# Optimization experiments

Measured on AMD Instinct MI355X. Metric: run time of the kernel, lower is better.

The kernel has to match this reference:

```python
import jax, jax.numpy as jnp
import numpy as np

EPS = 1e-13

def masked_softmax(x, mask):
    # Non-memory-efficient path of the original: softmax(x*mask), re-mask, renormalize.
    p = jax.nn.softmax(x * mask, axis=-1) * mask
    return p / (jnp.sum(p, axis=-1, keepdims=True) + EPS)

def setup_inputs() -> dict:
    key = jax.random.key(0)
    ka, kb, kma, kmb = jax.random.split(key, 4)
    B, La, Lb, D = 32, 1024, 1024, 256
    a = jax.random.normal(ka, (B, La, D), dtype=jnp.float32)
    b = jax.random.normal(kb, (B, Lb, D), dtype=jnp.float32)
    mask_a = jax.random.randint(kma, (B, La, 1), 0, 2, dtype=jnp.int32)
    mask_b = jax.random.randint(kmb, (B, Lb, 1), 0, 2, dtype=jnp.int32)
    return {"a": a, "b": b, "mask_a": mask_a, "mask_b": mask_b}

def reference(a, b, mask_a, mask_b):
    # a: [B, La, D], b: [B, Lb, D], mask_a: [B, La, 1], mask_b: [B, Lb, 1]
    ma = mask_a.astype(a.dtype)  # [B, La, 1]
    mb = mask_b.astype(b.dtype)  # [B, Lb, 1]
    attn = jnp.einsum('bid,bjd->bij', a, b)            # [B, La, Lb]
    amask = ma * jnp.swapaxes(mb, 1, 2)                 # outer product mask [B, La, Lb]
    weight_for_a = masked_softmax(attn, amask)          # softmax over Lb
    attended_a = jnp.einsum('bij,bjd->bid', weight_for_a, b)  # [B, La, D]
    attn_t = jnp.swapaxes(attn, 1, 2)                   # [B, Lb, La]
    amask_t = jnp.swapaxes(amask, 1, 2)
    weight_for_b = masked_softmax(attn_t, amask_t)      # softmax over La
    attended_b = jnp.einsum('bji,bid->bjd', weight_for_b, a)  # [B, Lb, D]
    return (attended_a, attended_b)
```

## Files before the change

### kernel.cpp

```cpp
#include <hip/hip_runtime.h>
#include <math.h>
#include <stdint.h>


#define NB    32
#define SEQ   1024
#define DIM   256
#define BM    128
#define BN    64
#define SHIFT 60.0f
#define PS    1048

typedef unsigned int uint;
typedef unsigned short ushort;
typedef __attribute__((ext_vector_type(8)))  short short8;
typedef __attribute__((ext_vector_type(16))) float f32x16;

#define KC_BATCH  (64 * 1024 * 8)
#define KC_TENSOR ((size_t)NB * KC_BATCH)
#define T_BATCH   (128 * 256 * 8)
#define T_TENSOR  ((size_t)NB * T_BATCH)
#define IDX_INTS  ((size_t)NB * SEQ)
#define WS_NEED   ((2 * KC_TENSOR + 2 * T_TENSOR) * sizeof(ushort) + (2 * IDX_INTS + 64) * sizeof(int))

__device__ __forceinline__ ushort bf16_rn(float x) {
    union { float f; uint u; } v; v.f = x;
    uint r = v.u + 0x7fffu + ((v.u >> 16) & 1u);
    return (ushort)(r >> 16);
}
__device__ __forceinline__ float bf16_to_f(ushort h) {
    union { uint u; float f; } v; v.u = ((uint)h) << 16;
    return v.f;
}
__device__ __forceinline__ void gl_lds16(const ushort* g, ushort* l) {
    __builtin_amdgcn_global_load_lds(
        (const __attribute__((address_space(1))) void*)g,
        (__attribute__((address_space(3))) void*)l, 16, 0, 0);
}

__global__ __launch_bounds__(1024)
void compact(const int* __restrict__ ma, const int* __restrict__ mb,
             int* __restrict__ idxA, int* __restrict__ idxB, int* __restrict__ nvArr)
{
    const int batch = blockIdx.x;
    const int t     = blockIdx.y;
    const int* m = t ? mb : ma;
    int* idx = (t ? idxB : idxA) + batch * SEQ;
    const int tid = threadIdx.x;
    const int lane = tid & 63, wv = tid >> 6;

    __shared__ int wsum[16];
    __shared__ int base[17];

    int v = (m[batch * SEQ + tid] != 0) ? 1 : 0;
    unsigned long long bal = __ballot(v);
    int lanePre = __popcll(bal & ((1ULL << lane) - 1ULL));
    if (lane == 0) wsum[wv] = __popcll(bal);
    __syncthreads();
    if (tid == 0) {
        int acc = 0;
        #pragma unroll
        for (int w = 0; w < 16; ++w) { base[w] = acc; acc += wsum[w]; }
        base[16] = acc;
        nvArr[t * NB + batch] = acc;
    }
    __syncthreads();
    if (v) idx[base[wv] + lanePre] = tid;
    if (tid >= base[16]) idx[tid] = 0;
}

__global__ __launch_bounds__(256)
void gatherK(const float* __restrict__ A, const float* __restrict__ Bt,
             const int* __restrict__ idxA, const int* __restrict__ idxB,
             const int* __restrict__ nvArr,
             ushort* __restrict__ aKc, ushort* __restrict__ bKc)
{
    const int z     = blockIdx.z;
    const int batch = blockIdx.y;
    const int soct  = blockIdx.x;
    const float* src = z ? Bt : A;
    const int* idx = (z ? idxB : idxA) + batch * SEQ;
    const int nv = nvArr[z * NB + batch];
    ushort* kcb = (z ? bKc : aKc) + (size_t)batch * KC_BATCH;

    const int tid = threadIdx.x;
    const int oct = tid >> 3, srow = tid & 7;
    const int c = soct * 8 + srow;

    float xs[8] = {0.f, 0.f, 0.f, 0.f, 0.f, 0.f, 0.f, 0.f};
    if (c < nv) {
        const float* rp = src + ((size_t)batch * SEQ + idx[c]) * DIM + oct * 8;
        float4 x0 = *(const float4*)rp;
        float4 x1 = *(const float4*)(rp + 4);
        xs[0]=x0.x; xs[1]=x0.y; xs[2]=x0.z; xs[3]=x0.w;
        xs[4]=x1.x; xs[5]=x1.y; xs[6]=x1.z; xs[7]=x1.w;
    }
    short8 hv, lv;
    #pragma unroll
    for (int j = 0; j < 8; ++j) {
        ushort h = bf16_rn(xs[j]);
        hv[j] = (short)h;
        lv[j] = (short)bf16_rn(xs[j] - bf16_to_f(h));
    }
    *(short8*)(kcb + (size_t)oct * 8192 + (size_t)c * 8)        = hv;
    *(short8*)(kcb + (size_t)(oct + 32) * 8192 + (size_t)c * 8) = lv;
}

__global__ __launch_bounds__(256)
void gatherT(const float* __restrict__ A, const float* __restrict__ Bt,
             const int* __restrict__ idxA, const int* __restrict__ idxB,
             const int* __restrict__ nvArr,
             ushort* __restrict__ aT, ushort* __restrict__ bT)
{
    const int z     = blockIdx.z;
    const int batch = blockIdx.y;
    const int soct  = blockIdx.x;
    const float* src = z ? Bt : A;
    const int* idx = (z ? idxB : idxA) + batch * SEQ;
    const int nv = nvArr[z * NB + batch];
    ushort* tp = (z ? bT : aT) + (size_t)batch * T_BATCH + (size_t)soct * 2048;
    const int d = threadIdx.x;
    short8 hv;
    #pragma unroll
    for (int j = 0; j < 8; ++j) {
        int c = soct * 8 + j;
        float x = 0.f;
        if (c < nv) x = src[((size_t)batch * SEQ + idx[c]) * DIM + d];
        hv[j] = (short)bf16_rn(x);
    }
    *(short8*)(tp + (size_t)d * 8) = hv;
}

__global__ __launch_bounds__(256)
void zeroOut(float4* __restrict__ p, int n4)
{
    int i = blockIdx.x * 256 + threadIdx.x;
    const int stride = gridDim.x * 256;
    const float4 z = {0.f, 0.f, 0.f, 0.f};
    for (; i < n4; i += stride) p[i] = z;
}

__global__ __launch_bounds__(512, 2)
void attend3(const ushort* __restrict__ aKc, const ushort* __restrict__ bKc,
             const ushort* __restrict__ aT,  const ushort* __restrict__ bT,
             const int*    __restrict__ idxA, const int* __restrict__ idxB,
             const int*    __restrict__ nvArr,
             float*        __restrict__ out)
{
    __shared__ __align__(16) ushort Ks2[64 * 512];
    __shared__ __align__(16) ushort Vt2[8 * 2048];
    __shared__ __align__(16) ushort Ph[8 * PS];
    __shared__ float lpart[2][BM];
    __shared__ float invs[BM];
    __shared__ int   oidx[BM];

    const int bx   = blockIdx.x;
    const int xcd  = bx & 7;
    const int slot = bx >> 3;
    const int rb   = slot & 7;
    const int pg   = slot >> 3;
    const int pair = xcd + 8 * pg;
    const int batch = pair >> 1;
    const int dir   = pair & 1;
    const int row0  = rb * BM;

    const ushort* qcY  = dir ? bKc  : aKc;
    const ushort* kcY  = dir ? aKc  : bKc;
    const ushort* tY   = dir ? aT   : bT;
    const int*    idxX = dir ? idxB : idxA;
    const int     nQ   = nvArr[(dir ? 1 : 0) * NB + batch];
    const int     nK   = nvArr[(dir ? 0 : 1) * NB + batch];
    const int     ntiles = (nK + BN - 1) >> 6;
    float* o = out + (size_t)dir * NB * SEQ * DIM;

    if (row0 >= nQ) return;

    const int tid  = threadIdx.x;
    const int lane = tid & 63;
    const int wave = tid >> 6;
    const int l31  = lane & 31;
    const int lh   = lane >> 5;
    const int rw   = wave >> 1;
    const int cw   = wave & 1;

    const ushort* qcYb = qcY + (size_t)batch * KC_BATCH;
    const ushort* kcYb = kcY + (size_t)batch * KC_BATCH;
    const ushort* tYb  = tY  + (size_t)batch * T_BATCH;

    const ushort* ksrc = kcYb + (size_t)(wave * 8) * 8192 + (size_t)lane * 8;
    ushort*       kdst = Ks2 + wave * 8 * 512 + lane * 8;
    const ushort* vsrc = tYb + (size_t)wave * 2048 + (size_t)lane * 8;
    ushort*       vdst = Vt2 + wave * 2048 + lane * 8;

    #pragma unroll
    for (int i = 0; i < 8; ++i) gl_lds16(ksrc + (size_t)i * 8192, kdst + i * 512);
    #pragma unroll
    for (int i = 0; i < 4; ++i) gl_lds16(vsrc + i * 512, vdst + i * 512);

    const int qrow = row0 + rw * 32 + l31;
    short8 qhi[16], qlo[16];
    {
        const ushort* qb = qcYb + (size_t)lh * 8192 + (size_t)qrow * 8;
        #pragma unroll
        for (int kk = 0; kk < 16; ++kk) {
            qhi[kk] = *(const short8*)(qb + (size_t)(2 * kk) * 8192);
            qlo[kk] = *(const short8*)(qb + (size_t)(2 * kk + 32) * 8192);
        }
    }

    f32x16 oacc[4];
    #pragma unroll
    for (int t = 0; t < 4; ++t)
        #pragma unroll
        for (int r = 0; r < 16; ++r) oacc[t][r] = 0.f;
    float lsum[16];
    #pragma unroll
    for (int r = 0; r < 16; ++r) lsum[r] = 0.f;

    __syncthreads();

    for (int nt = 0; nt < ntiles; ++nt) {
        const int key0 = nt * BN;
        const float mkv = (key0 + cw * 32 + l31 < nK) ? 1.f : 0.f;

        f32x16 a1, a2;
        #pragma unroll
        for (int r = 0; r < 16; ++r) { a1[r] = 0.f; a2[r] = 0.f; }
        const int kcol = (cw * 32 + l31) * 8;
        #pragma unroll
        for (int kk = 0; kk < 16; ++kk) {
            short8 bhi = *(const short8*)&Ks2[(2 * kk + lh) * 512 + kcol];
            a1 = __builtin_amdgcn_mfma_f32_32x32x16_bf16(qhi[kk], bhi, a1, 0, 0, 0);
            a2 = __builtin_amdgcn_mfma_f32_32x32x16_bf16(qlo[kk], bhi, a2, 0, 0, 0);
        }
        #pragma unroll
        for (int kk = 0; kk < 16; ++kk) {
            short8 blo = *(const short8*)&Ks2[(2 * kk + lh + 32) * 512 + kcol];
            a2 = __builtin_amdgcn_mfma_f32_32x32x16_bf16(qhi[kk], blo, a2, 0, 0, 0);
        }

        const int key  = cw * 32 + l31;
        const int koct = key >> 3, kj = key & 7;
        #pragma unroll
        for (int r = 0; r < 16; ++r) {
            float s = a1[r] + a2[r];
            float p = __expf(s - SHIFT) * mkv;
            lsum[r] += p;
            int qr = rw * 32 + (r & 3) + ((r >> 2) << 3) + (lh << 2);
            Ph[koct * PS + qr * 8 + kj] = bf16_rn(p);
        }
        __syncthreads();

        if (nt + 1 < ntiles) {
            const ushort* ks = ksrc + (size_t)(key0 + BN) * 8;
            #pragma unroll
            for (int i = 0; i < 8; ++i) gl_lds16(ks + (size_t)i * 8192, kdst + i * 512);
        }

        const int prow = (rw * 32 + l31) * 8;
        #pragma unroll
        for (int kb = 0; kb < 4; ++kb) {
            short8 pa = *(const short8*)&Ph[(2 * kb + lh) * PS + prow];
            #pragma unroll
            for (int t = 0; t < 4; ++t) {
                int dim = cw * 128 + t * 32 + l31;
                short8 vf = *(const short8*)&Vt2[(2 * kb + lh) * 2048 + dim * 8];
                oacc[t] = __builtin_amdgcn_mfma_f32_32x32x16_bf16(pa, vf, oacc[t], 0, 0, 0);
            }
        }
        __syncthreads();

        if (nt + 1 < ntiles) {
            const ushort* vs = vsrc + ((size_t)(key0 + BN) >> 3) * 2048;
            #pragma unroll
            for (int i = 0; i < 4; ++i) gl_lds16(vs + i * 512, vdst + i * 512);
        }
    }

    #pragma unroll
    for (int r = 0; r < 16; ++r) {
        float v = lsum[r];
        v += __shfl_xor(v, 1, 64);
        v += __shfl_xor(v, 2, 64);
        v += __shfl_xor(v, 4, 64);
        v += __shfl_xor(v, 8, 64);
        v += __shfl_xor(v, 16, 64);
        if (l31 == 0) {
            int row = rw * 32 + (r & 3) + ((r >> 2) << 3) + (lh << 2);
            lpart[cw][row] = v;
        }
    }
    __syncthreads();
    if (tid < BM) {
        int crow = row0 + tid;
        float l = lpart[0][tid] + lpart[1][tid];
        int valid = (crow < nQ);
        invs[tid] = (valid && l > 0.f) ? 1.f / l : 0.f;
        oidx[tid] = valid ? idxX[batch * SEQ + crow] : 0;
    }
    __syncthreads();

    float* ob = o + (size_t)batch * SEQ * DIM;
    #pragma unroll
    for (int r = 0; r < 16; ++r) {
        int rloc = rw * 32 + (r & 3) + ((r >> 2) << 3) + (lh << 2);
        float inv = invs[rloc];
        if (inv != 0.f) {
            int orow = oidx[rloc];
            #pragma unroll
            for (int t = 0; t < 4; ++t) {
                int d = cw * 128 + t * 32 + l31;
                ob[(size_t)orow * DIM + d] = oacc[t][r] * inv;
            }
        }
    }
}

#define F_KS_STR 520
#define F_P_STR  136
#define F_BM 64
#define F_BN 64
__global__ __launch_bounds__(256, 1)
void attend_mfma(const float* __restrict__ X, const float* __restrict__ Y,
                 const int* __restrict__ mx, const int* __restrict__ my,
                 float* __restrict__ out)
{
    __shared__ ushort Ks[F_BN * F_KS_STR];
    __shared__ ushort Ps[F_BM * F_P_STR];
    __shared__ float  mk[F_BN];
    __shared__ float  lpart[2][F_BM];
    __shared__ float  invs[F_BM];

    const int tid = threadIdx.x, lane = tid & 63, wave = tid >> 6;
    const int l31 = lane & 31, lh = lane >> 5;
    const int rw = wave >> 1, cw = wave & 1;
    const int batch = blockIdx.y, row0 = blockIdx.x * F_BM;
    const float* Xb = X + (size_t)batch * SEQ * DIM;
    const float* Yb = Y + (size_t)batch * SEQ * DIM;

    float4 kreg[16]; int mreg = 0;
    #pragma unroll
    for (int i = 0; i < 16; ++i) {
        int idx = tid + (i << 8); int r = idx >> 6, c4 = idx & 63;
        kreg[i] = *((const float4*)(Yb + (size_t)r * DIM) + c4);
    }
    if (tid < F_BN) mreg = my[batch * SEQ + tid];

    short8 qhi[16], qlo[16];
    {
        const float* qrow = Xb + (size_t)(row0 + rw * 32 + l31) * DIM + lh * 8;
        #pragma unroll
        for (int kk = 0; kk < 16; ++kk) {
            const float* p = qrow + kk * 16;
            float4 x0 = *(const float4*)p; float4 x1 = *(const float4*)(p + 4);
            float xs[8] = {x0.x, x0.y, x0.z, x0.w, x1.x, x1.y, x1.z, x1.w};
            #pragma unroll
            for (int j = 0; j < 8; ++j) {
                ushort h = bf16_rn(xs[j]);
                qhi[kk][j] = (short)h;
                qlo[kk][j] = (short)bf16_rn(xs[j] - bf16_to_f(h));
            }
        }
    }
    f32x16 oacc[4];
    #pragma unroll
    for (int t = 0; t < 4; ++t)
        #pragma unroll
        for (int r = 0; r < 16; ++r) oacc[t][r] = 0.f;
    float lsum[16];
    #pragma unroll
    for (int r = 0; r < 16; ++r) lsum[r] = 0.f;

    for (int nt = 0; nt < SEQ / F_BN; ++nt) {
        if (nt) __syncthreads();
        #pragma unroll
        for (int i = 0; i < 16; ++i) {
            int idx = tid + (i << 8); int r = idx >> 6, c4 = idx & 63;
            float f[4] = {kreg[i].x, kreg[i].y, kreg[i].z, kreg[i].w};
            ushort hh[4], ll[4];
            #pragma unroll
            for (int q = 0; q < 4; ++q) { hh[q] = bf16_rn(f[q]); ll[q] = bf16_rn(f[q] - bf16_to_f(hh[q])); }
            ushort4 hv; hv.x=hh[0];hv.y=hh[1];hv.z=hh[2];hv.w=hh[3];
            ushort4 lv; lv.x=ll[0];lv.y=ll[1];lv.z=ll[2];lv.w=ll[3];
            *(ushort4*)&Ks[r * F_KS_STR + c4 * 4] = hv;
            *(ushort4*)&Ks[r * F_KS_STR + 256 + c4 * 4] = lv;
        }
        if (tid < F_BN) mk[tid] = (float)mreg;
        __syncthreads();
        if (nt + 1 < SEQ / F_BN) {
            const float* Ybn = Yb + (size_t)(nt + 1) * F_BN * DIM;
            #pragma unroll
            for (int i = 0; i < 16; ++i) {
                int idx = tid + (i << 8); int r = idx >> 6, c4 = idx & 63;
                kreg[i] = *((const float4*)(Ybn + (size_t)r * DIM) + c4);
            }
            if (tid < F_BN) mreg = my[batch * SEQ + (nt + 1) * F_BN + tid];
        }
        f32x16 a1, a2, a3;
        #pragma unroll
        for (int r = 0; r < 16; ++r) { a1[r]=0.f; a2[r]=0.f; a3[r]=0.f; }
        const int krow = (cw * 32 + l31) * F_KS_STR;
        #pragma unroll
        for (int kk = 0; kk < 16; ++kk) {
            int col = kk * 16 + lh * 8;
            short8 bhi = *(const short8*)&Ks[krow + col];
            short8 blo = *(const short8*)&Ks[krow + 256 + col];
            a1 = __builtin_amdgcn_mfma_f32_32x32x16_bf16(qhi[kk], bhi, a1, 0, 0, 0);
            a2 = __builtin_amdgcn_mfma_f32_32x32x16_bf16(qlo[kk], bhi, a2, 0, 0, 0);
            a3 = __builtin_amdgcn_mfma_f32_32x32x16_bf16(qhi[kk], blo, a3, 0, 0, 0);
        }
        const float mkv = mk[cw * 32 + l31];
        #pragma unroll
        for (int r = 0; r < 16; ++r) {
            float s = a1[r] + a2[r] + a3[r];
            float p = __expf(s - SHIFT) * mkv;
            lsum[r] += p;
            ushort ph = bf16_rn(p);
            ushort pl = bf16_rn(p - bf16_to_f(ph));
            int prow = rw * 32 + (r & 3) + ((r >> 2) << 3) + (lh << 2);
            int pcol = cw * 32 + l31;
            Ps[prow * F_P_STR + pcol] = ph;
            Ps[prow * F_P_STR + 64 + pcol] = pl;
        }
        __syncthreads();
        const int prow = (rw * 32 + l31) * F_P_STR;
        #pragma unroll
        for (int kb = 0; kb < 4; ++kb) {
            int pcol = kb * 16 + lh * 8;
            short8 pa_hi = *(const short8*)&Ps[prow + pcol];
            short8 pa_lo = *(const short8*)&Ps[prow + 64 + pcol];
            #pragma unroll
            for (int t = 0; t < 4; ++t) {
                int d0 = cw * 128 + t * 32 + l31;
                short8 vf;
                #pragma unroll
                for (int j = 0; j < 8; ++j) vf[j] = (short)Ks[(pcol + j) * F_KS_STR + d0];
                oacc[t] = __builtin_amdgcn_mfma_f32_32x32x16_bf16(pa_hi, vf, oacc[t], 0, 0, 0);
                oacc[t] = __builtin_amdgcn_mfma_f32_32x32x16_bf16(pa_lo, vf, oacc[t], 0, 0, 0);
            }
        }
    }
    #pragma unroll
    for (int r = 0; r < 16; ++r) {
        float v = lsum[r];
        v += __shfl_xor(v, 1, 64); v += __shfl_xor(v, 2, 64); v += __shfl_xor(v, 4, 64);
        v += __shfl_xor(v, 8, 64); v += __shfl_xor(v, 16, 64);
        if (l31 == 0) {
            int row = rw * 32 + (r & 3) + ((r >> 2) << 3) + (lh << 2);
            lpart[cw][row] = v;
        }
    }
    __syncthreads();
    if (tid < F_BM) {
        float l = lpart[0][tid] + lpart[1][tid];
        int valid = mx[batch * SEQ + row0 + tid];
        invs[tid] = (valid != 0 && l > 0.f) ? 1.f / l : 0.f;
    }
    __syncthreads();
    float* ob = out + ((size_t)batch * SEQ + row0) * DIM;
    #pragma unroll
    for (int r = 0; r < 16; ++r) {
        int rloc = rw * 32 + (r & 3) + ((r >> 2) << 3) + (lh << 2);
        float inv = invs[rloc];
        #pragma unroll
        for (int t = 0; t < 4; ++t) {
            int d = cw * 128 + t * 32 + l31;
            ob[(size_t)rloc * DIM + d] = oacc[t][r] * inv;
        }
    }
}

extern "C" void kernel_launch(void* const* d_in, const int* in_sizes, int n_in,
                              void* d_out, int out_size, void* d_ws, size_t ws_size,
                              hipStream_t stream) {
    const float* a  = (const float*)d_in[0];
    const float* b  = (const float*)d_in[1];
    const int*   ma = (const int*)d_in[2];
    const int*   mb = (const int*)d_in[3];
    float* out = (float*)d_out;

    if (ws_size >= WS_NEED) {
        ushort* wsu = (ushort*)d_ws;
        ushort* aKc = wsu;
        ushort* bKc = wsu + KC_TENSOR;
        ushort* aT  = wsu + 2 * KC_TENSOR;
        ushort* bT  = wsu + 2 * KC_TENSOR + T_TENSOR;
        int* idxA  = (int*)(wsu + 2 * KC_TENSOR + 2 * T_TENSOR);
        int* idxB  = idxA + IDX_INTS;
        int* nvArr = idxB + IDX_INTS;

        compact<<<dim3(NB, 2), 1024, 0, stream>>>(ma, mb, idxA, idxB, nvArr);
        gatherK<<<dim3(128, NB, 2), 256, 0, stream>>>(a, b, idxA, idxB, nvArr, aKc, bKc);
        gatherT<<<dim3(128, NB, 2), 256, 0, stream>>>(a, b, idxA, idxB, nvArr, aT, bT);
        zeroOut<<<dim3(2048), 256, 0, stream>>>((float4*)out, out_size / 16);
        attend3<<<dim3(512, 1, 1), 512, 0, stream>>>(aKc, bKc, aT, bT,
                                                     idxA, idxB, nvArr, out);
    } else {
        float* out_a = out;
        float* out_b = out + (size_t)NB * SEQ * DIM;
        dim3 grid(SEQ / F_BM, NB), block(256);
        attend_mfma<<<grid, block, 0, stream>>>(a, b, ma, mb, out_a);
        attend_mfma<<<grid, block, 0, stream>>>(b, a, mb, ma, out_b);
    }
}
```

Before: 281.9 us.

## Fuse gather kernels via LDS transpose and zero masked rows inside attention

Merges the two gather kernels into one that loads each source row once, writes the hi/lo bf16 split, and stages the floats in shared memory to emit the transposed bf16 copy. Blocks beyond the padded valid count now exit early. The separate full-output zeroing kernel is dropped: the attention kernel instead zeros only the output rows whose query mask is zero. This removes two launches, a second read of the inputs, and most of the output memset traffic, at the cost of extra shared memory and a barrier in the gather.

```diff
diff --git a/kernel.cpp b/kernel.cpp
--- a/kernel.cpp
+++ b/kernel.cpp
@@ -69,11 +69,13 @@
     if (tid >= base[16]) idx[tid] = 0;
 }
 
+#define GSTR 264
 __global__ __launch_bounds__(256)
-void gatherK(const float* __restrict__ A, const float* __restrict__ Bt,
-             const int* __restrict__ idxA, const int* __restrict__ idxB,
-             const int* __restrict__ nvArr,
-             ushort* __restrict__ aKc, ushort* __restrict__ bKc)
+void gatherKT(const float* __restrict__ A, const float* __restrict__ Bt,
+              const int* __restrict__ idxA, const int* __restrict__ idxB,
+              const int* __restrict__ nvArr,
+              ushort* __restrict__ aKc, ushort* __restrict__ bKc,
+              ushort* __restrict__ aT,  ushort* __restrict__ bT)
 {
     const int z     = blockIdx.z;
     const int batch = blockIdx.y;
@@ -81,7 +83,13 @@
     const float* src = z ? Bt : A;
     const int* idx = (z ? idxB : idxA) + batch * SEQ;
     const int nv = nvArr[z * NB + batch];
+    const int ntr = (nv + 63) & ~63;
+    if (soct * 8 >= ntr) return;
+
     ushort* kcb = (z ? bKc : aKc) + (size_t)batch * KC_BATCH;
+    ushort* tp  = ((z ? bT : aT) + (size_t)batch * T_BATCH) + (size_t)soct * 2048;
+
+    __shared__ float tile[8 * GSTR];
 
     const int tid = threadIdx.x;
     const int oct = tid >> 3, srow = tid & 7;
@@ -101,43 +109,20 @@
         ushort h = bf16_rn(xs[j]);
         hv[j] = (short)h;
         lv[j] = (short)bf16_rn(xs[j] - bf16_to_f(h));
+        tile[srow * GSTR + oct * 8 + j] = xs[j];
     }
     *(short8*)(kcb + (size_t)oct * 8192 + (size_t)c * 8)        = hv;
     *(short8*)(kcb + (size_t)(oct + 32) * 8192 + (size_t)c * 8) = lv;
-}
-
-__global__ __launch_bounds__(256)
-void gatherT(const float* __restrict__ A, const float* __restrict__ Bt,
-             const int* __restrict__ idxA, const int* __restrict__ idxB,
-             const int* __restrict__ nvArr,
-             ushort* __restrict__ aT, ushort* __restrict__ bT)
-{
-    const int z     = blockIdx.z;
-    const int batch = blockIdx.y;
-    const int soct  = blockIdx.x;
-    const float* src = z ? Bt : A;
-    const int* idx = (z ? idxB : idxA) + batch * SEQ;
-    const int nv = nvArr[z * NB + batch];
-    ushort* tp = (z ? bT : aT) + (size_t)batch * T_BATCH + (size_t)soct * 2048;
-    const int d = threadIdx.x;
-    short8 hv;
-    #pragma unroll
-    for (int j = 0; j < 8; ++j) {
-        int c = soct * 8 + j;
-        float x = 0.f;
-        if (c < nv) x = src[((size_t)batch * SEQ + idx[c]) * DIM + d];
-        hv[j] = (short)bf16_rn(x);
-    }
-    *(short8*)(tp + (size_t)d * 8) = hv;
-}
-
-__global__ __launch_bounds__(256)
-void zeroOut(float4* __restrict__ p, int n4)
-{
-    int i = blockIdx.x * 256 + threadIdx.x;
-    const int stride = gridDim.x * 256;
-    const float4 z = {0.f, 0.f, 0.f, 0.f};
-    for (; i < n4; i += stride) p[i] = z;
+
+    __syncthreads();
+    {
+        const int d = tid;
+        short8 tv;
+        #pragma unroll
+        for (int j = 0; j < 8; ++j)
+            tv[j] = (short)bf16_rn(tile[j * GSTR + d]);
+        *(short8*)(tp + (size_t)d * 8) = tv;
+    }
 }
 
 __global__ __launch_bounds__(512, 2)
@@ -145,6 +130,7 @@
              const ushort* __restrict__ aT,  const ushort* __restrict__ bT,
              const int*    __restrict__ idxA, const int* __restrict__ idxB,
              const int*    __restrict__ nvArr,
+             const int*    __restrict__ ma,  const int*    __restrict__ mb,
              float*        __restrict__ out)
 {
     __shared__ __align__(16) ushort Ks2[64 * 512];
@@ -168,14 +154,27 @@
     const ushort* kcY  = dir ? aKc  : bKc;
     const ushort* tY   = dir ? aT   : bT;
     const int*    idxX = dir ? idxB : idxA;
+    const int*    mq   = dir ? mb   : ma;
     const int     nQ   = nvArr[(dir ? 1 : 0) * NB + batch];
     const int     nK   = nvArr[(dir ? 0 : 1) * NB + batch];
     const int     ntiles = (nK + BN - 1) >> 6;
     float* o = out + (size_t)dir * NB * SEQ * DIM;
 
+    const int tid  = threadIdx.x;
+
+    {
+        float* ob0 = o + (size_t)batch * SEQ * DIM;
+        const int orow = rb * BM + (tid >> 2);
+        if (mq[batch * SEQ + orow] == 0) {
+            float4* p = (float4*)(ob0 + (size_t)orow * DIM + (tid & 3) * 64);
+            const float4 zz = {0.f, 0.f, 0.f, 0.f};
+            #pragma unroll
+            for (int i = 0; i < 16; ++i) p[i] = zz;
+        }
+    }
+
     if (row0 >= nQ) return;
 
-    const int tid  = threadIdx.x;
     const int lane = tid & 63;
     const int wave = tid >> 6;
     const int l31  = lane & 31;
@@ -490,11 +489,10 @@
         int* nvArr = idxB + IDX_INTS;
 
         compact<<<dim3(NB, 2), 1024, 0, stream>>>(ma, mb, idxA, idxB, nvArr);
-        gatherK<<<dim3(128, NB, 2), 256, 0, stream>>>(a, b, idxA, idxB, nvArr, aKc, bKc);
-        gatherT<<<dim3(128, NB, 2), 256, 0, stream>>>(a, b, idxA, idxB, nvArr, aT, bT);
-        zeroOut<<<dim3(2048), 256, 0, stream>>>((float4*)out, out_size / 16);
+        gatherKT<<<dim3(128, NB, 2), 256, 0, stream>>>(a, b, idxA, idxB, nvArr,
+                                                       aKc, bKc, aT, bT);
         attend3<<<dim3(512, 1, 1), 512, 0, stream>>>(aKc, bKc, aT, bT,
-                                                     idxA, idxB, nvArr, out);
+                                                     idxA, idxB, nvArr, ma, mb, out);
     } else {
         float* out_a = out;
         float* out_b = out + (size_t)NB * SEQ * DIM;
```

Result: faster. 271.0 us (-3.9%).
